# Optimization experiments

Measured on AMD Instinct MI355X. Metric: run time of the kernel, lower is better.

Reference implementation:

```python
import jax, jax.numpy as jnp
import numpy as np

HIDDEN = 1024
N_HEAD = 16
HEAD_DIM = HIDDEN // N_HEAD  # 64
BATCH = 1
SEQ = 4096
THETA = 10000.0


def _rope_cos_sin(seq_len, head_dim, dtype=jnp.float32):
    # freqs[t, j] = t / theta^(2j/dim), j in [0, dim/2)
    inv_freq = 1.0 / (THETA ** (jnp.arange(0, head_dim, 2, dtype=dtype) / head_dim))
    t = jnp.arange(seq_len, dtype=dtype)
    freqs = jnp.outer(t, inv_freq)           # [S, D/2]
    return jnp.cos(freqs), jnp.sin(freqs)


def _apply_rope(x, cos, sin):
    # x: [B, S, H, D]; pairs (x[...,2j], x[...,2j+1]) rotated by angle freqs[t, j]
    x2 = x.reshape(*x.shape[:-1], -1, 2)       # [B, S, H, D/2, 2]
    x_re, x_im = x2[..., 0], x2[..., 1]
    c = cos[None, :, None, :]                   # [1, S, 1, D/2]
    s = sin[None, :, None, :]
    out_re = x_re * c - x_im * s
    out_im = x_re * s + x_im * c
    out = jnp.stack([out_re, out_im], axis=-1)  # [B, S, H, D/2, 2]
    return out.reshape(x.shape)


def setup_inputs() -> dict:
    key = jax.random.key(0)
    kx, kq, kk, kv = jax.random.split(key, 4)
    scale = 1.0 / np.sqrt(HIDDEN)
    return {
        "x": jax.random.normal(kx, (BATCH, SEQ, HIDDEN), dtype=jnp.float32),
        "wq": jax.random.normal(kq, (HIDDEN, HIDDEN), dtype=jnp.float32) * scale,
        "wk": jax.random.normal(kk, (HIDDEN, HIDDEN), dtype=jnp.float32) * scale,
        "wv": jax.random.normal(kv, (HIDDEN, HIDDEN), dtype=jnp.float32) * scale,
    }


def reference(x, wq, wk, wv):
    B, S, _ = x.shape
    # torch nn.Linear(no bias): y = x @ W.T
    xq = (x @ wq.T).reshape(B, S, N_HEAD, HEAD_DIM).astype(jnp.float32)
    xk = (x @ wk.T).reshape(B, S, N_HEAD, HEAD_DIM).astype(jnp.float32)
    xv = (x @ wv.T).reshape(B, S, N_HEAD, HEAD_DIM).astype(jnp.float32)

    cos, sin = _rope_cos_sin(S, HEAD_DIM)
    q = _apply_rope(xq, cos, sin)
    k = _apply_rope(xk, cos, sin)

    # [B, H, S, S] scores, no causal mask (matches source)
    scores = jnp.einsum("bqhd,bkhd->bhqk", q, k) / jnp.sqrt(
        jnp.asarray(HEAD_DIM, dtype=q.dtype))
    attn = jax.nn.softmax(scores, axis=-1)
    out = jnp.einsum("bhqk,bkhd->bqhd", attn, xv)  # [B, S, H, D]
    return out.reshape(B, S, N_HEAD * HEAD_DIM)
```

## Files before the change

kernel.cpp:

```cpp
#include <hip/hip_runtime.h>
#include <stdint.h>


#define SEQLEN 4096
#define NHEAD 16
#define HDIM 64

typedef __bf16 bf16x8 __attribute__((ext_vector_type(8)));
typedef float f32x4 __attribute__((ext_vector_type(4)));
typedef float f32x16 __attribute__((ext_vector_type(16)));

__device__ __forceinline__ unsigned short f2bf(float f) {
  union { float f; unsigned int u; } v; v.f = f;
  unsigned int r = v.u + 0x7FFFu + ((v.u >> 16) & 1u);
  return (unsigned short)(r >> 16);
}
__device__ __forceinline__ unsigned int pkc(float lo, float hi) {
  union { __bf16 b[2]; unsigned int u; } z;
  z.b[0] = (__bf16)lo; z.b[1] = (__bf16)hi;
  return z.u;
}
__device__ __forceinline__ bf16x8 as_bf(uint4 v) { return __builtin_bit_cast(bf16x8, v); }
__device__ __forceinline__ f32x4 mfma16(bf16x8 a, bf16x8 b, f32x4 c) {
  return __builtin_amdgcn_mfma_f32_16x16x32_bf16(a, b, c, 0, 0, 0);
}
__device__ __forceinline__ f32x16 mfma32(bf16x8 a, bf16x8 b, f32x16 c) {
  return __builtin_amdgcn_mfma_f32_32x32x16_bf16(a, b, c, 0, 0, 0);
}

__global__ __launch_bounds__(256) void k_convert(
    const float* __restrict__ x, const float* __restrict__ wq,
    const float* __restrict__ wk, const float* __restrict__ wv,
    unsigned short* __restrict__ xbf, unsigned short* __restrict__ wbf) {
  int i = blockIdx.x * 256 + threadIdx.x;
  const int NX = SEQLEN * 1024 / 4;
  const int NW = 1024 * 1024 / 4;
  float4 v;
  unsigned short* dst;
  int di;
  if (i < NX) {
    v = ((const float4*)x)[i]; dst = xbf; di = i;
  } else {
    int j = i - NX;
    const float4* src = (const float4*)((j < NW) ? wq : (j < 2 * NW) ? wk : wv);
    v = src[j & (NW - 1)];
    dst = wbf; di = j;
  }
  ushort4 o; o.x = f2bf(v.x); o.y = f2bf(v.y); o.z = f2bf(v.z); o.w = f2bf(v.w);
  ((ushort4*)dst)[di] = o;
}

__global__ __launch_bounds__(256) void k_table(float* __restrict__ ct, float* __restrict__ st) {
  int i = blockIdx.x * 256 + threadIdx.x;
  int s = i >> 5, j = i & 31;
  double inv = exp(-(double)j * 0.28782313662425572);
  double a = (double)s * inv;
  ct[i] = (float)cos(a);
  st[i] = (float)sin(a);
}

__global__ __launch_bounds__(256) void k_gemm(
    const unsigned short* __restrict__ xbf, const unsigned short* __restrict__ wbf,
    const float* __restrict__ ct, const float* __restrict__ st,
    unsigned short* __restrict__ qbf, unsigned short* __restrict__ kbf,
    unsigned short* __restrict__ vT) {
  __shared__ __align__(16) unsigned short As[2][128 * 40];
  __shared__ __align__(16) unsigned short Bs[2][128 * 40];
  const int t = threadIdx.x;
  const int bn = blockIdx.x, bm = blockIdx.y;
  const int lane = t & 63, wave = t >> 6;
  const int r = lane & 15, g = lane >> 4;
  const int wm = wave >> 1, wn = wave & 1;

  const int c0 = t, c1 = t + 256;
  const int ar0 = c0 >> 2, ao0 = (c0 & 3) * 16;
  const int ar1 = c1 >> 2, ao1 = (c1 & 3) * 16;
  const char* Ab = (const char*)xbf;
  const char* Bb = (const char*)wbf;

  uint4 ra0, ra1, rb0, rb1;
#define LD_TILE(kk)                                                             \
  ra0 = *(const uint4*)(Ab + (size_t)(bm * 128 + ar0) * 2048 + (kk) * 64 + ao0); \
  ra1 = *(const uint4*)(Ab + (size_t)(bm * 128 + ar1) * 2048 + (kk) * 64 + ao1); \
  rb0 = *(const uint4*)(Bb + (size_t)(bn * 128 + ar0) * 2048 + (kk) * 64 + ao0); \
  rb1 = *(const uint4*)(Bb + (size_t)(bn * 128 + ar1) * 2048 + (kk) * 64 + ao1);

  LD_TILE(0)
  f32x4 zero4 = {0.f, 0.f, 0.f, 0.f};
  f32x4 acc[4][4];
#pragma unroll
  for (int m = 0; m < 4; ++m)
#pragma unroll
    for (int n = 0; n < 4; ++n) acc[m][n] = zero4;

  for (int kk = 0; kk < 32; ++kk) {
    unsigned short* Ac = As[kk & 1];
    unsigned short* Bc = Bs[kk & 1];
    *(uint4*)((char*)Ac + ar0 * 80 + ao0) = ra0;
    *(uint4*)((char*)Ac + ar1 * 80 + ao1) = ra1;
    *(uint4*)((char*)Bc + ar0 * 80 + ao0) = rb0;
    *(uint4*)((char*)Bc + ar1 * 80 + ao1) = rb1;
    __syncthreads();
    if (kk < 31) { LD_TILE(kk + 1) }
    bf16x8 af[4], bfr[4];
#pragma unroll
    for (int m = 0; m < 4; ++m)
      af[m] = as_bf(*(const uint4*)((const char*)Ac + (wm * 64 + m * 16 + r) * 80 + g * 16));
#pragma unroll
    for (int n = 0; n < 4; ++n)
      bfr[n] = as_bf(*(const uint4*)((const char*)Bc + (wn * 64 + n * 16 + r) * 80 + g * 16));
#pragma unroll
    for (int m = 0; m < 4; ++m)
#pragma unroll
      for (int n = 0; n < 4; ++n)
        acc[m][n] = mfma16(af[m], bfr[n], acc[m][n]);
  }

  const int matid = bn >> 3;
#pragma unroll
  for (int m = 0; m < 4; ++m) {
    const int row0 = bm * 128 + wm * 64 + m * 16 + 4 * g;
#pragma unroll
    for (int n = 0; n < 4; ++n) {
      const int col = bn * 128 + wn * 64 + n * 16 + r;
      const int d = col & 63;
      const int hh = (col >> 6) & 15;
      if (matid < 2) {
        const int jdx = (col >> 1) & 31;
        const float sgn = (col & 1) ? 1.0f : -1.0f;
        unsigned short* dst = (matid == 0) ? qbf : kbf;
        const float qs = (matid == 0) ? 0.18033688011112042f : 1.0f;
#pragma unroll
        for (int j = 0; j < 4; ++j) {
          float v = acc[m][n][j];
          float p = __shfl_xor(v, 1);
          int srow = row0 + j;
          float cv = ct[srow * 32 + jdx];
          float sv = st[srow * 32 + jdx];
          float o = (v * cv + p * sv * sgn) * qs;
          dst[(size_t)srow * 1024 + (hh * 64 + d)] = f2bf(o);
        }
      } else {
        ushort4 o;
        o.x = f2bf(acc[m][n][0]); o.y = f2bf(acc[m][n][1]);
        o.z = f2bf(acc[m][n][2]); o.w = f2bf(acc[m][n][3]);
        *(ushort4*)&vT[((size_t)(hh * 64 + d)) * SEQLEN + row0] = o;
      }
    }
  }
}

__global__ __launch_bounds__(512) void k_attn(
    const unsigned short* __restrict__ qbf, const unsigned short* __restrict__ kbf,
    const unsigned short* __restrict__ vT, float* __restrict__ out) {
  __shared__ __align__(16) char smem[65536];
  const int t = threadIdx.x;
  const int b = blockIdx.x;
  const int work = (b & 7) * 64 + (b >> 3);
  const int h = work >> 5;
  const int qb = work & 31;
  const int lane = t & 63, wave = t >> 6;
  const int qw = wave & 3, hf = wave >> 2;
  const int li = lane & 31, hi = lane >> 5;
  const int q0 = qb * 128 + qw * 32;

  bf16x8 qf[4];
#pragma unroll
  for (int c = 0; c < 4; ++c)
    qf[c] = as_bf(*(const uint4*)((const char*)qbf +
              (size_t)(q0 + li) * 2048 + h * 128 + c * 32 + hi * 16));

  f32x16 z16 = {0.f};
  f32x16 acc[2];
  acc[0] = z16; acc[1] = z16;
  f32x16 accL = z16;

  uint4 onesu; onesu.x = 0x3F803F80u; onesu.y = 0x3F803F80u;
  onesu.z = 0x3F803F80u; onesu.w = 0x3F803F80u;
  const bf16x8 ones8 = as_bf(onesu);

  const int tt = t & 255;
  const int srow = tt >> 2, sbyte = (tt & 3) * 16;
  const int swz = (srow & 7) << 4;
  const int wa0 = srow * 128 + (sbyte ^ swz);
  const int wa1 = srow * 128 + ((sbyte + 64) ^ swz);
  const char* kg = (const char*)kbf + h * 128;
  const char* vg = (const char*)vT + (size_t)h * HDIM * SEQLEN * 2;
  char* base = smem + hf * 32768;

  uint4 rk0, rk1, rv0, rv1;
#define LD_KV64(kt)                                                            \
  rk0 = *(const uint4*)(kg + (size_t)((kt) * 64 + srow) * 2048 + sbyte);       \
  rk1 = *(const uint4*)(kg + (size_t)((kt) * 64 + srow) * 2048 + sbyte + 64);  \
  rv0 = *(const uint4*)(vg + (size_t)srow * 8192 + (kt) * 128 + sbyte);        \
  rv1 = *(const uint4*)(vg + (size_t)srow * 8192 + (kt) * 128 + sbyte + 64);

  LD_KV64(hf * 32)

  const int frsw = (lane & 7) << 4;

  for (int j = 0; j < 32; ++j) {
    char* Kb = base + (j & 1) * 8192;
    char* Vb = base + 16384 + (j & 1) * 8192;
    *(uint4*)(Kb + wa0) = rk0;
    *(uint4*)(Kb + wa1) = rk1;
    *(uint4*)(Vb + wa0) = rv0;
    *(uint4*)(Vb + wa1) = rv1;
    __syncthreads();
    if (j < 31) { LD_KV64(hf * 32 + j + 1) }

    f32x16 sT[2];
    sT[0] = z16; sT[1] = z16;
    __builtin_amdgcn_s_setprio(1);
#pragma unroll
    for (int c = 0; c < 4; ++c) {
      const int co = (((2 * c + hi) * 16) ^ frsw);
      bf16x8 k0 = as_bf(*(const uint4*)(Kb + li * 128 + co));
      bf16x8 k1 = as_bf(*(const uint4*)(Kb + (32 + li) * 128 + co));
      sT[0] = mfma32(k0, qf[c], sT[0]);
      sT[1] = mfma32(k1, qf[c], sT[1]);
    }
    __builtin_amdgcn_s_setprio(0);

    bf16x8 vf[2][4];
#pragma unroll
    for (int dt = 0; dt < 2; ++dt) {
      const int vrow = (dt * 32 + li) * 128;
#pragma unroll
      for (int kc = 0; kc < 4; ++kc) {
        uint2 vlo = *(const uint2*)(Vb + vrow + (((kc * 32) ^ frsw) + hi * 8));
        uint2 vhi = *(const uint2*)(Vb + vrow + (((kc * 32 + 16) ^ frsw) + hi * 8));
        uint4 vv; vv.x = vlo.x; vv.y = vlo.y; vv.z = vhi.x; vv.w = vhi.y;
        vf[dt][kc] = as_bf(vv);
      }
    }

#pragma unroll
    for (int s = 0; s < 2; ++s)
#pragma unroll
      for (int i = 0; i < 16; ++i) sT[s][i] = __builtin_amdgcn_exp2f(sT[s][i]);

#pragma unroll
    for (int kc = 0; kc < 4; ++kc) {
      const int sub = kc >> 1, bix = (kc & 1) * 8;
      uint4 bw;
      bw.x = pkc(sT[sub][bix + 0], sT[sub][bix + 1]);
      bw.y = pkc(sT[sub][bix + 2], sT[sub][bix + 3]);
      bw.z = pkc(sT[sub][bix + 4], sT[sub][bix + 5]);
      bw.w = pkc(sT[sub][bix + 6], sT[sub][bix + 7]);
      bf16x8 pfr = as_bf(bw);
      __builtin_amdgcn_s_setprio(1);
      acc[0] = mfma32(vf[0][kc], pfr, acc[0]);
      acc[1] = mfma32(vf[1][kc], pfr, acc[1]);
      accL = mfma32(ones8, pfr, accL);
      __builtin_amdgcn_s_setprio(0);
    }
  }

  float lhalf = accL[0];

  __syncthreads();
  float* shm = (float*)smem;
  if (hf == 1) {
    float* ab = shm + qw * 2048;
#pragma unroll
    for (int dt = 0; dt < 2; ++dt)
#pragma unroll
      for (int i = 0; i < 16; ++i) {
        int d = (i & 3) + 8 * (i >> 2) + 4 * hi + 32 * dt;
        ab[d * 32 + li] = acc[dt][i];
      }
    if (hi == 0) shm[8192 + qw * 32 + li] = lhalf;
  }
  __syncthreads();
  if (hf == 0) {
    float* ab = shm + qw * 2048;
    float l1 = shm[8192 + qw * 32 + li];
    float linv = 1.0f / (lhalf + l1);
#pragma unroll
    for (int dt = 0; dt < 2; ++dt)
#pragma unroll
      for (int i = 0; i < 16; ++i) {
        int d = (i & 3) + 8 * (i >> 2) + 4 * hi + 32 * dt;
        acc[dt][i] = (acc[dt][i] + ab[d * 32 + li]) * linv;
      }
    __asm__ volatile("" ::: "memory");

    float* eb = shm + qw * 2048;
#pragma unroll
    for (int dt = 0; dt < 2; ++dt) {
#pragma unroll
      for (int i = 0; i < 16; ++i)
        eb[li * 33 + ((i & 3) + 8 * (i >> 2) + 4 * hi)] = acc[dt][i];
      __asm__ volatile("" ::: "memory");
#pragma unroll
      for (int it = 0; it < 16; ++it) {
        int q = it * 2 + hi;
        float v = eb[q * 33 + li];
        out[(size_t)(q0 + q) * 1024 + h * 64 + dt * 32 + li] = v;
      }
      __asm__ volatile("" ::: "memory");
    }
  }
}

extern "C" void kernel_launch(void* const* d_in, const int* in_sizes, int n_in,
                              void* d_out, int out_size, void* d_ws, size_t ws_size,
                              hipStream_t stream) {
  const float* x  = (const float*)d_in[0];
  const float* wq = (const float*)d_in[1];
  const float* wk = (const float*)d_in[2];
  const float* wv = (const float*)d_in[3];
  float* out = (float*)d_out;
  char* ws = (char*)d_ws;

  unsigned short* qbf = (unsigned short*)(ws);
  unsigned short* kbf = (unsigned short*)(ws + ((size_t)8 << 20));
  unsigned short* vT  = (unsigned short*)(ws + ((size_t)16 << 20));
  unsigned short* xbf = (unsigned short*)(ws + ((size_t)24 << 20));
  unsigned short* wbf = (unsigned short*)(ws + ((size_t)32 << 20));
  float* ct = (float*)(ws + ((size_t)38 << 20));
  float* st = (float*)(ws + ((size_t)38 << 20) + ((size_t)512 << 10));

  k_convert<<<dim3(7168), dim3(256), 0, stream>>>(x, wq, wk, wv, xbf, wbf);
  k_table<<<dim3(512), dim3(256), 0, stream>>>(ct, st);
  k_gemm<<<dim3(24, 32), dim3(256), 0, stream>>>(xbf, wbf, ct, st, qbf, kbf, vT);
  k_attn<<<dim3(512), dim3(512), 0, stream>>>(qbf, kbf, vT, out);
}
```

Before: 160.7 us.

## Drop KV split in attention; one 4-wave block covers full key range

The attention kernel previously split the key sequence across two wave groups (512 threads), then merged partial accumulators and row sums through shared memory. It now uses 256 threads per block, with each wave looping over all 64 key tiles, which removes the cross-half reduction and halves shared memory. The PV MFMAs are also grouped after all P fragments are packed, under a single priority window. The trade-off is half the waves per block and a loop twice as long, so there is less latency hiding per block but potentially more blocks resident per CU.

```diff
diff --git a/kernel.cpp b/kernel.cpp
--- a/kernel.cpp
+++ b/kernel.cpp
@@ -150,17 +150,16 @@
   }
 }
 
-__global__ __launch_bounds__(512) void k_attn(
+__global__ __launch_bounds__(256) void k_attn(
     const unsigned short* __restrict__ qbf, const unsigned short* __restrict__ kbf,
     const unsigned short* __restrict__ vT, float* __restrict__ out) {
-  __shared__ __align__(16) char smem[65536];
+  __shared__ __align__(16) char smem[32768];
   const int t = threadIdx.x;
   const int b = blockIdx.x;
   const int work = (b & 7) * 64 + (b >> 3);
   const int h = work >> 5;
   const int qb = work & 31;
-  const int lane = t & 63, wave = t >> 6;
-  const int qw = wave & 3, hf = wave >> 2;
+  const int lane = t & 63, qw = t >> 6;
   const int li = lane & 31, hi = lane >> 5;
   const int q0 = qb * 128 + qw * 32;
 
@@ -179,14 +178,12 @@
   onesu.z = 0x3F803F80u; onesu.w = 0x3F803F80u;
   const bf16x8 ones8 = as_bf(onesu);
 
-  const int tt = t & 255;
-  const int srow = tt >> 2, sbyte = (tt & 3) * 16;
+  const int srow = t >> 2, sbyte = (t & 3) * 16;
   const int swz = (srow & 7) << 4;
   const int wa0 = srow * 128 + (sbyte ^ swz);
   const int wa1 = srow * 128 + ((sbyte + 64) ^ swz);
   const char* kg = (const char*)kbf + h * 128;
   const char* vg = (const char*)vT + (size_t)h * HDIM * SEQLEN * 2;
-  char* base = smem + hf * 32768;
 
   uint4 rk0, rk1, rv0, rv1;
 #define LD_KV64(kt)                                                            \
@@ -195,19 +192,19 @@
   rv0 = *(const uint4*)(vg + (size_t)srow * 8192 + (kt) * 128 + sbyte);        \
   rv1 = *(const uint4*)(vg + (size_t)srow * 8192 + (kt) * 128 + sbyte + 64);
 
-  LD_KV64(hf * 32)
+  LD_KV64(0)
 
   const int frsw = (lane & 7) << 4;
 
-  for (int j = 0; j < 32; ++j) {
-    char* Kb = base + (j & 1) * 8192;
-    char* Vb = base + 16384 + (j & 1) * 8192;
+  for (int j = 0; j < 64; ++j) {
+    char* Kb = smem + (j & 1) * 8192;
+    char* Vb = smem + 16384 + (j & 1) * 8192;
     *(uint4*)(Kb + wa0) = rk0;
     *(uint4*)(Kb + wa1) = rk1;
     *(uint4*)(Vb + wa0) = rv0;
     *(uint4*)(Vb + wa1) = rv1;
     __syncthreads();
-    if (j < 31) { LD_KV64(hf * 32 + j + 1) }
+    if (j < 63) { LD_KV64(j + 1) }
 
     f32x16 sT[2];
     sT[0] = z16; sT[1] = z16;
@@ -240,6 +237,7 @@
 #pragma unroll
       for (int i = 0; i < 16; ++i) sT[s][i] = __builtin_amdgcn_exp2f(sT[s][i]);
 
+    bf16x8 pfr[4];
 #pragma unroll
     for (int kc = 0; kc < 4; ++kc) {
       const int sub = kc >> 1, bix = (kc & 1) * 8;
@@ -248,59 +246,35 @@
       bw.y = pkc(sT[sub][bix + 2], sT[sub][bix + 3]);
       bw.z = pkc(sT[sub][bix + 4], sT[sub][bix + 5]);
       bw.w = pkc(sT[sub][bix + 6], sT[sub][bix + 7]);
-      bf16x8 pfr = as_bf(bw);
-      __builtin_amdgcn_s_setprio(1);
-      acc[0] = mfma32(vf[0][kc], pfr, acc[0]);
-      acc[1] = mfma32(vf[1][kc], pfr, acc[1]);
-      accL = mfma32(ones8, pfr, accL);
-      __builtin_amdgcn_s_setprio(0);
-    }
-  }
-
-  float lhalf = accL[0];
+      pfr[kc] = as_bf(bw);
+    }
+    __builtin_amdgcn_s_setprio(1);
+#pragma unroll
+    for (int kc = 0; kc < 4; ++kc) {
+      acc[0] = mfma32(vf[0][kc], pfr[kc], acc[0]);
+      acc[1] = mfma32(vf[1][kc], pfr[kc], acc[1]);
+      accL = mfma32(ones8, pfr[kc], accL);
+    }
+    __builtin_amdgcn_s_setprio(0);
+  }
+
+  float linv = 1.0f / accL[0];
 
   __syncthreads();
-  float* shm = (float*)smem;
-  if (hf == 1) {
-    float* ab = shm + qw * 2048;
-#pragma unroll
-    for (int dt = 0; dt < 2; ++dt)
-#pragma unroll
-      for (int i = 0; i < 16; ++i) {
-        int d = (i & 3) + 8 * (i >> 2) + 4 * hi + 32 * dt;
-        ab[d * 32 + li] = acc[dt][i];
-      }
-    if (hi == 0) shm[8192 + qw * 32 + li] = lhalf;
-  }
-  __syncthreads();
-  if (hf == 0) {
-    float* ab = shm + qw * 2048;
-    float l1 = shm[8192 + qw * 32 + li];
-    float linv = 1.0f / (lhalf + l1);
-#pragma unroll
-    for (int dt = 0; dt < 2; ++dt)
-#pragma unroll
-      for (int i = 0; i < 16; ++i) {
-        int d = (i & 3) + 8 * (i >> 2) + 4 * hi + 32 * dt;
-        acc[dt][i] = (acc[dt][i] + ab[d * 32 + li]) * linv;
-      }
+  float* eb = (float*)smem + qw * 1056;
+#pragma unroll
+  for (int dt = 0; dt < 2; ++dt) {
+#pragma unroll
+    for (int i = 0; i < 16; ++i)
+      eb[li * 33 + ((i & 3) + 8 * (i >> 2) + 4 * hi)] = acc[dt][i] * linv;
     __asm__ volatile("" ::: "memory");
-
-    float* eb = shm + qw * 2048;
-#pragma unroll
-    for (int dt = 0; dt < 2; ++dt) {
-#pragma unroll
-      for (int i = 0; i < 16; ++i)
-        eb[li * 33 + ((i & 3) + 8 * (i >> 2) + 4 * hi)] = acc[dt][i];
-      __asm__ volatile("" ::: "memory");
-#pragma unroll
-      for (int it = 0; it < 16; ++it) {
-        int q = it * 2 + hi;
-        float v = eb[q * 33 + li];
-        out[(size_t)(q0 + q) * 1024 + h * 64 + dt * 32 + li] = v;
-      }
-      __asm__ volatile("" ::: "memory");
-    }
+#pragma unroll
+    for (int it = 0; it < 16; ++it) {
+      int q = it * 2 + hi;
+      float v = eb[q * 33 + li];
+      out[(size_t)(q0 + q) * 1024 + h * 64 + dt * 32 + li] = v;
+    }
+    __asm__ volatile("" ::: "memory");
   }
 }
 
@@ -325,5 +299,5 @@
   k_convert<<<dim3(7168), dim3(256), 0, stream>>>(x, wq, wk, wv, xbf, wbf);
   k_table<<<dim3(512), dim3(256), 0, stream>>>(ct, st);
   k_gemm<<<dim3(24, 32), dim3(256), 0, stream>>>(xbf, wbf, ct, st, qbf, kbf, vT);
-  k_attn<<<dim3(512), dim3(512), 0, stream>>>(qbf, kbf, vT, out);
-}
+  k_attn<<<dim3(512), dim3(256), 0, stream>>>(qbf, kbf, vT, out);
+}
```

Result: slower. 170.3 us (+6.0%).

## Replace ones-MFMA row sum with VALU reduction and re-swizzle LDS tiles

Applied to the files above, without the earlier changes.

The softmax denominator was computed with an extra MFMA against a vector of ones. It is now summed from the exponentiated fp32 scores with VALU adds, followed by one cross-half shuffle, which removes a third of the PV-stage MFMAs. The LDS layout switches to an 8-byte-granularity XOR swizzle with precomputed per-lane read and write addresses, and all P fragments are packed before the MFMA burst. The loop is also unrolled by two. The sum now uses fp32 values rather than bf16-rounded P, which slightly changes numerics. The narrower LDS accesses may add instruction count.

```diff
diff --git a/kernel.cpp b/kernel.cpp
--- a/kernel.cpp
+++ b/kernel.cpp
@@ -26,6 +26,9 @@
 }
 __device__ __forceinline__ f32x16 mfma32(bf16x8 a, bf16x8 b, f32x16 c) {
   return __builtin_amdgcn_mfma_f32_32x32x16_bf16(a, b, c, 0, 0, 0);
+}
+__device__ __forceinline__ uint2 mku2(unsigned x, unsigned y) {
+  uint2 r; r.x = x; r.y = y; return r;
 }
 
 __global__ __launch_bounds__(256) void k_convert(
@@ -163,6 +166,7 @@
   const int qw = wave & 3, hf = wave >> 2;
   const int li = lane & 31, hi = lane >> 5;
   const int q0 = qb * 128 + qw * 32;
+  const int HB = hf * 32768;
 
   bf16x8 qf[4];
 #pragma unroll
@@ -173,39 +177,56 @@
   f32x16 z16 = {0.f};
   f32x16 acc[2];
   acc[0] = z16; acc[1] = z16;
-  f32x16 accL = z16;
-
-  uint4 onesu; onesu.x = 0x3F803F80u; onesu.y = 0x3F803F80u;
-  onesu.z = 0x3F803F80u; onesu.w = 0x3F803F80u;
-  const bf16x8 ones8 = as_bf(onesu);
-
+  float lrun = 0.f;
+
+  const int m4 = li & 15;
+  const int mmK = m4 ^ (hi << 1);
+  const int mmV = m4 ^ hi;
+  int kra[4][2];
+#pragma unroll
+  for (int c = 0; c < 4; ++c) {
+    int s0 = (4 * c) ^ mmK;
+    kra[c][0] = HB + li * 128 + (s0 << 3);
+    kra[c][1] = HB + li * 128 + ((s0 ^ 1) << 3);
+  }
+  int vra[4][2];
+#pragma unroll
+  for (int kc = 0; kc < 4; ++kc) {
+    int s0 = (4 * kc) ^ mmV;
+    vra[kc][0] = HB + 16384 + li * 128 + (s0 << 3);
+    vra[kc][1] = HB + 16384 + li * 128 + ((s0 ^ 2) << 3);
+  }
   const int tt = t & 255;
-  const int srow = tt >> 2, sbyte = (tt & 3) * 16;
-  const int swz = (srow & 7) << 4;
-  const int wa0 = srow * 128 + (sbyte ^ swz);
-  const int wa1 = srow * 128 + ((sbyte + 64) ^ swz);
+  const int srow = tt >> 2, chunk = tt & 3;
+  const int wm4 = srow & 15;
+  int wa[4];
+#pragma unroll
+  for (int j = 0; j < 4; ++j)
+    wa[j] = HB + srow * 128 + (((chunk * 4 + j) ^ wm4) << 3);
+
   const char* kg = (const char*)kbf + h * 128;
   const char* vg = (const char*)vT + (size_t)h * HDIM * SEQLEN * 2;
-  char* base = smem + hf * 32768;
 
   uint4 rk0, rk1, rv0, rv1;
-#define LD_KV64(kt)                                                            \
-  rk0 = *(const uint4*)(kg + (size_t)((kt) * 64 + srow) * 2048 + sbyte);       \
-  rk1 = *(const uint4*)(kg + (size_t)((kt) * 64 + srow) * 2048 + sbyte + 64);  \
-  rv0 = *(const uint4*)(vg + (size_t)srow * 8192 + (kt) * 128 + sbyte);        \
-  rv1 = *(const uint4*)(vg + (size_t)srow * 8192 + (kt) * 128 + sbyte + 64);
+#define LD_KV64(kt)                                                                 \
+  rk0 = *(const uint4*)(kg + (size_t)((kt) * 64 + srow) * 2048 + chunk * 32);       \
+  rk1 = *(const uint4*)(kg + (size_t)((kt) * 64 + srow) * 2048 + chunk * 32 + 16);  \
+  rv0 = *(const uint4*)(vg + (size_t)srow * 8192 + (kt) * 128 + chunk * 32);        \
+  rv1 = *(const uint4*)(vg + (size_t)srow * 8192 + (kt) * 128 + chunk * 32 + 16);
 
   LD_KV64(hf * 32)
 
-  const int frsw = (lane & 7) << 4;
-
+#pragma unroll 2
   for (int j = 0; j < 32; ++j) {
-    char* Kb = base + (j & 1) * 8192;
-    char* Vb = base + 16384 + (j & 1) * 8192;
-    *(uint4*)(Kb + wa0) = rk0;
-    *(uint4*)(Kb + wa1) = rk1;
-    *(uint4*)(Vb + wa0) = rv0;
-    *(uint4*)(Vb + wa1) = rv1;
+    const int JB = (j & 1) * 8192;
+    *(uint2*)(smem + wa[0] + JB) = mku2(rk0.x, rk0.y);
+    *(uint2*)(smem + wa[1] + JB) = mku2(rk0.z, rk0.w);
+    *(uint2*)(smem + wa[2] + JB) = mku2(rk1.x, rk1.y);
+    *(uint2*)(smem + wa[3] + JB) = mku2(rk1.z, rk1.w);
+    *(uint2*)(smem + wa[0] + 16384 + JB) = mku2(rv0.x, rv0.y);
+    *(uint2*)(smem + wa[1] + 16384 + JB) = mku2(rv0.z, rv0.w);
+    *(uint2*)(smem + wa[2] + 16384 + JB) = mku2(rv1.x, rv1.y);
+    *(uint2*)(smem + wa[3] + 16384 + JB) = mku2(rv1.z, rv1.w);
     __syncthreads();
     if (j < 31) { LD_KV64(hf * 32 + j + 1) }
 
@@ -214,32 +235,44 @@
     __builtin_amdgcn_s_setprio(1);
 #pragma unroll
     for (int c = 0; c < 4; ++c) {
-      const int co = (((2 * c + hi) * 16) ^ frsw);
-      bf16x8 k0 = as_bf(*(const uint4*)(Kb + li * 128 + co));
-      bf16x8 k1 = as_bf(*(const uint4*)(Kb + (32 + li) * 128 + co));
-      sT[0] = mfma32(k0, qf[c], sT[0]);
-      sT[1] = mfma32(k1, qf[c], sT[1]);
+      uint2 a0 = *(const uint2*)(smem + kra[c][0] + JB);
+      uint2 a1 = *(const uint2*)(smem + kra[c][1] + JB);
+      uint2 b0 = *(const uint2*)(smem + kra[c][0] + JB + 4096);
+      uint2 b1 = *(const uint2*)(smem + kra[c][1] + JB + 4096);
+      uint4 k0u; k0u.x = a0.x; k0u.y = a0.y; k0u.z = a1.x; k0u.w = a1.y;
+      uint4 k1u; k1u.x = b0.x; k1u.y = b0.y; k1u.z = b1.x; k1u.w = b1.y;
+      sT[0] = mfma32(as_bf(k0u), qf[c], sT[0]);
+      sT[1] = mfma32(as_bf(k1u), qf[c], sT[1]);
     }
     __builtin_amdgcn_s_setprio(0);
 
     bf16x8 vf[2][4];
 #pragma unroll
-    for (int dt = 0; dt < 2; ++dt) {
-      const int vrow = (dt * 32 + li) * 128;
+    for (int dt = 0; dt < 2; ++dt)
 #pragma unroll
       for (int kc = 0; kc < 4; ++kc) {
-        uint2 vlo = *(const uint2*)(Vb + vrow + (((kc * 32) ^ frsw) + hi * 8));
-        uint2 vhi = *(const uint2*)(Vb + vrow + (((kc * 32 + 16) ^ frsw) + hi * 8));
-        uint4 vv; vv.x = vlo.x; vv.y = vlo.y; vv.z = vhi.x; vv.w = vhi.y;
+        uint2 lo = *(const uint2*)(smem + vra[kc][0] + JB + dt * 4096);
+        uint2 hi2 = *(const uint2*)(smem + vra[kc][1] + JB + dt * 4096);
+        uint4 vv; vv.x = lo.x; vv.y = lo.y; vv.z = hi2.x; vv.w = hi2.y;
         vf[dt][kc] = as_bf(vv);
       }
-    }
 
 #pragma unroll
     for (int s = 0; s < 2; ++s)
 #pragma unroll
       for (int i = 0; i < 16; ++i) sT[s][i] = __builtin_amdgcn_exp2f(sT[s][i]);
 
+    float sum8[8];
+#pragma unroll
+    for (int i = 0; i < 8; ++i) sum8[i] = (sT[0][i] + sT[0][i + 8]) + (sT[1][i] + sT[1][i + 8]);
+#pragma unroll
+    for (int sft = 4; sft >= 1; sft >>= 1)
+#pragma unroll
+      for (int i = 0; i < 4; ++i)
+        if (i < sft) sum8[i] += sum8[i + sft];
+    lrun += sum8[0];
+
+    bf16x8 pfr[4];
 #pragma unroll
     for (int kc = 0; kc < 4; ++kc) {
       const int sub = kc >> 1, bix = (kc & 1) * 8;
@@ -248,16 +281,18 @@
       bw.y = pkc(sT[sub][bix + 2], sT[sub][bix + 3]);
       bw.z = pkc(sT[sub][bix + 4], sT[sub][bix + 5]);
       bw.w = pkc(sT[sub][bix + 6], sT[sub][bix + 7]);
-      bf16x8 pfr = as_bf(bw);
-      __builtin_amdgcn_s_setprio(1);
-      acc[0] = mfma32(vf[0][kc], pfr, acc[0]);
-      acc[1] = mfma32(vf[1][kc], pfr, acc[1]);
-      accL = mfma32(ones8, pfr, accL);
-      __builtin_amdgcn_s_setprio(0);
-    }
-  }
-
-  float lhalf = accL[0];
+      pfr[kc] = as_bf(bw);
+    }
+    __builtin_amdgcn_s_setprio(1);
+#pragma unroll
+    for (int kc = 0; kc < 4; ++kc) {
+      acc[0] = mfma32(vf[0][kc], pfr[kc], acc[0]);
+      acc[1] = mfma32(vf[1][kc], pfr[kc], acc[1]);
+    }
+    __builtin_amdgcn_s_setprio(0);
+  }
+
+  float lhalf = lrun + __shfl_xor(lrun, 32);
 
   __syncthreads();
   float* shm = (float*)smem;
```

New measurement: 151.2 us. 5.9% less time.
